# Optimization experiments

Measured on AMD Instinct MI355X. Metric: run time of the kernel, lower is better.

## Reference

```python
import jax, jax.numpy as jnp
import numpy as np

H, DK, DV, CHUNK = 4, 256, 256, 32
MIN_FLOOR, MAX_FLOOR, TEMP_MIN = 0.01, 0.1, 0.5


def _silu(x):
    return x * jax.nn.sigmoid(x)


def _causal_dw_conv(x_bcl, w_ck):
    # depthwise causal 1-D conv: x (b, C, L), w (C, K)
    K = w_ck.shape[-1]
    return jax.lax.conv_general_dilated(
        x_bcl, w_ck[:, None, :], window_strides=(1,), padding=[(K - 1, 0)],
        feature_group_count=x_bcl.shape[1])


def _l2norm(x):
    return x * jax.lax.rsqrt(jnp.sum(x * x, axis=-1, keepdims=True) + 1e-6)


def _delta_rule_chunkwise(q, k, v, beta, chunk=CHUNK):
    # q,k: (b,h,L,dk)  v: (b,h,L,dv)  beta: (b,h,L); L divisible by chunk
    b, h, L, dk = q.shape
    dv = v.shape[-1]
    n = L // chunk
    q = _l2norm(q)
    k = _l2norm(k)
    v = v * beta[..., None]
    kb = k * beta[..., None]
    qc, kc, vc, kbc = (t.reshape(b, h, n, chunk, -1) for t in (q, k, v, kb))
    # in-chunk inverse: the torch row loop computes (I + tril(k_beta k^T, -1))^{-1}
    A = jnp.einsum('bhncd,bhned->bhnce', kbc, kc)
    eye = jnp.eye(chunk, dtype=q.dtype)
    T = eye + jnp.tril(A, -1)
    inv = jax.scipy.linalg.solve_triangular(
        T, jnp.broadcast_to(eye, T.shape), lower=True, unit_diagonal=True)
    u = inv @ vc      # (b,h,n,c,dv)
    w = inv @ kbc     # (b,h,n,c,dk)
    strict = jnp.triu(jnp.ones((chunk, chunk), dtype=bool), 1)

    def step(S, xs):
        q_i, k_i, u_i, w_i = xs
        att = jnp.where(strict, 0.0, jnp.einsum('bhcd,bhed->bhce', q_i, k_i))
        u_adj = u_i - jnp.einsum('bhck,bhkd->bhcd', w_i, S)
        o = jnp.einsum('bhck,bhkd->bhcd', q_i, S) + att @ u_adj
        S = S + jnp.einsum('bhck,bhcd->bhkd', k_i, u_adj)
        return S, o

    mv = lambda t: jnp.moveaxis(t, 2, 0)  # chunks to scan axis
    S0 = jnp.zeros((b, h, dk, dv), dtype=q.dtype)
    S, outs = jax.lax.scan(step, S0, (mv(qc), mv(kc), mv(u), mv(w)))
    out = jnp.moveaxis(outs, 0, 2).reshape(b, h, L, dv)
    return out, S


def _fir(x, filt):
    # x: (b,l,h,d), filt: (h,d,K) depthwise causal FIR per (head, channel)
    b, l, h, d = x.shape
    xc = x.transpose(0, 2, 3, 1).reshape(b, h * d, l)
    y = _causal_dw_conv(xc, filt.reshape(h * d, -1))
    return y.reshape(b, h, d, l).transpose(0, 3, 1, 2)


def setup_inputs() -> dict:
    key = jax.random.key(0)
    ks = iter(jax.random.split(key, 32))
    B, L, D = 4, 2048, 1024
    kd, vd = H * DK, H * DV
    rn = lambda shp, s=0.02: jax.random.normal(next(ks), shp, jnp.float32) * s
    fir = lambda K: (jnp.zeros((H, DV, K), jnp.float32).at[..., -1].set(1.0)
                     + 0.01 * jax.random.normal(next(ks), (H, DV, K), jnp.float32))
    return dict(
        hidden_states=jax.random.normal(next(ks), (B, L, D), jnp.float32),
        Wq=rn((D, kd)), Wk=rn((D, kd)), Wv=rn((D, vd)),
        q_conv_w=rn((kd, 4), 0.3), k_conv_w=rn((kd, 4), 0.3), v_conv_w=rn((vd, 4), 0.3),
        Wb=rn((D, H)),
        fir_w3=fir(3), fir_w7=fir(7), fir_w15=fir(15), fir_w31=fir(31),
        router_W1=rn((D + DV * H * 5, 2 * D)), router_b1=jnp.zeros((2 * D,), jnp.float32),
        router_W2=rn((2 * D, H * 5)), router_b2=jnp.zeros((H * 5,), jnp.float32),
        id_gate_W=rn((D, H)), id_gate_b=jnp.full((H,), 2.0, jnp.float32),
        log_tau=jnp.zeros((H,), jnp.float32),
        o_norm_w=jnp.ones((DV,), jnp.float32),
        Wo=rn((vd, D)))


def reference(hidden_states, Wq, Wk, Wv, q_conv_w, k_conv_w, v_conv_w, Wb,
              fir_w3, fir_w7, fir_w15, fir_w31,
              router_W1, router_b1, router_W2, router_b2,
              id_gate_W, id_gate_b, log_tau, o_norm_w, Wo):
    B, L, D = hidden_states.shape
    conv = lambda x, w: _silu(_causal_dw_conv(x.transpose(0, 2, 1), w)).transpose(0, 2, 1)
    q = conv(hidden_states @ Wq, q_conv_w).reshape(B, L, H, DK)
    k = conv(hidden_states @ Wk, k_conv_w).reshape(B, L, H, DK)
    v_direct = conv(hidden_states @ Wv, v_conv_w).reshape(B, L, H, DV)
    beta = jax.nn.sigmoid(hidden_states @ Wb)  # (B,L,H)
    delta_out, _ = _delta_rule_chunkwise(
        q.transpose(0, 2, 1, 3), k.transpose(0, 2, 1, 3),
        v_direct.transpose(0, 2, 1, 3), beta.transpose(0, 2, 1))
    delta_out = delta_out.transpose(0, 2, 1, 3)  # (B,L,H,DV)
    paths = [_fir(v_direct, f) for f in (fir_w3, fir_w7, fir_w15, fir_w31)] + [delta_out]
    # token-adaptive value/context split
    p_value = jax.nn.sigmoid(hidden_states @ id_gate_W + id_gate_b)  # (B,L,H)
    floor_tok = MIN_FLOOR + (MAX_FLOOR - MIN_FLOOR) * (1.0 - p_value)
    p_value_adj = (1.0 - floor_tok) * p_value
    context_mass = 1.0 - p_value_adj
    # router over [hidden, all context paths]
    router_in = jnp.concatenate(
        [hidden_states] + [p.reshape(B, L, H * DV) for p in paths], axis=-1)
    hmid = jax.nn.gelu(router_in @ router_W1 + router_b1, approximate=False)
    logits = (hmid @ router_W2 + router_b2).reshape(B, L, H, 5)
    tau = jnp.maximum(jnp.exp(log_tau), TEMP_MIN)  # (H,)
    probs = jax.nn.softmax(logits / tau[:, None], axis=-1)
    ctx = sum(probs[..., i:i + 1] * paths[i] for i in range(5))
    o = context_mass[..., None] * ctx + p_value_adj[..., None] * v_direct
    # per-head RMSNorm then output projection
    o = o * jax.lax.rsqrt(jnp.mean(o * o, axis=-1, keepdims=True) + 1e-5) * o_norm_w
    return o.reshape(B, L, H * DV) @ Wo
```

## Files before the change

kernel.cpp:

```cpp
#include <hip/hip_runtime.h>
#include <math.h>

#define NTOK   8192
#define LSEQ   2048
#define NCHUNK 64

typedef short bhalf8 __attribute__((ext_vector_type(8)));
typedef float floatx4 __attribute__((ext_vector_type(4)));

__device__ inline ushort f2bf(float f) {
  uint u = __float_as_uint(f);
  u += 0x7FFFu + ((u >> 16) & 1u);
  return (ushort)(u >> 16);
}
__device__ inline float bf2f(ushort h) {
  return __uint_as_float(((uint)h) << 16);
}

#define GLD_LDS16(g, s) __builtin_amdgcn_global_load_lds(                      \
    (const __attribute__((address_space(1))) void*)(g),                        \
    (__attribute__((address_space(3))) void*)(s), 16, 0, 0)

__global__ __launch_bounds__(256)
void cvt_bf16(const float* __restrict__ x, ushort* __restrict__ y, int n8) {
  int i = blockIdx.x * 256 + threadIdx.x;
  if (i >= n8) return;
  const float4* xp = (const float4*)x;
  float4 a = xp[2 * i], b = xp[2 * i + 1];
  uint4 o;
  o.x = (uint)f2bf(a.x) | ((uint)f2bf(a.y) << 16);
  o.y = (uint)f2bf(a.z) | ((uint)f2bf(a.w) << 16);
  o.z = (uint)f2bf(b.x) | ((uint)f2bf(b.y) << 16);
  o.w = (uint)f2bf(b.z) | ((uint)f2bf(b.w) << 16);
  ((uint4*)y)[i] = o;
}

__global__ __launch_bounds__(256)
void cvt_t(const float* __restrict__ x, ushort* __restrict__ y, int R, int C) {
  __shared__ float tile[32][33];
  int r0 = blockIdx.y * 32, c0 = blockIdx.x * 32;
  int tr = threadIdx.x >> 5;
  int tc = threadIdx.x & 31;
  #pragma unroll
  for (int rr = tr; rr < 32; rr += 8)
    tile[rr][tc] = x[(size_t)(r0 + rr) * C + c0 + tc];
  __syncthreads();
  #pragma unroll
  for (int rr = tr; rr < 32; rr += 8)
    y[(size_t)(c0 + rr) * R + r0 + tc] = f2bf(tile[tc][rr]);
}

template<int ACC>
__global__ __launch_bounds__(256)
void gemm_bf(const ushort* __restrict__ A, const ushort* __restrict__ BT,
             float* __restrict__ C, int K, int lda, int ldbt, int ldc) {
  __shared__ ushort Asm[128 * 32];
  __shared__ ushort Bsm[128 * 32];
  const int t = threadIdx.x;
  const int w = t >> 6, l = t & 63;
  const int m0 = blockIdx.y * 128, n0 = blockIdx.x * 128;
  const int wr = w >> 1, wc = w & 1;
  const int srow = l >> 2;
  const int sgc  = (l & 3) ^ ((l >> 3) & 3);
  const int ridx = (l & 15) * 32 + (((l >> 4) ^ ((l >> 1) & 3)) * 8);

  floatx4 acc[4][4];
  #pragma unroll
  for (int i = 0; i < 4; i++)
    #pragma unroll
    for (int j = 0; j < 4; j++)
      #pragma unroll
      for (int r = 0; r < 4; r++) acc[i][j][r] = 0.f;

  for (int k0 = 0; k0 < K; k0 += 32) {
    __syncthreads();
    #pragma unroll
    for (int j = 0; j < 2; j++) {
      int sub = w * 2 + j;
      GLD_LDS16(A + (size_t)(m0 + sub * 16 + srow) * lda + k0 + sgc * 8,
                Asm + sub * 512);
      GLD_LDS16(BT + (size_t)(n0 + sub * 16 + srow) * ldbt + k0 + sgc * 8,
                Bsm + sub * 512);
    }
    __syncthreads();
    bhalf8 af[4], bf_[4];
    #pragma unroll
    for (int i = 0; i < 4; i++)
      af[i] = *(const bhalf8*)&Asm[(wr * 4 + i) * 512 + ridx];
    #pragma unroll
    for (int j = 0; j < 4; j++)
      bf_[j] = *(const bhalf8*)&Bsm[(wc * 4 + j) * 512 + ridx];
    #pragma unroll
    for (int i = 0; i < 4; i++)
      #pragma unroll
      for (int j = 0; j < 4; j++)
        acc[i][j] = __builtin_amdgcn_mfma_f32_16x16x32_bf16(af[i], bf_[j],
                                                            acc[i][j], 0, 0, 0);
  }
  const int crow = (l >> 4) * 4;
  const int ccol = l & 15;
  #pragma unroll
  for (int i = 0; i < 4; i++)
    #pragma unroll
    for (int j = 0; j < 4; j++) {
      float* cp = &C[(size_t)(m0 + wr * 64 + i * 16 + crow) * ldc +
                     n0 + wc * 64 + j * 16 + ccol];
      #pragma unroll
      for (int r = 0; r < 4; r++) {
        if (ACC) cp[(size_t)r * ldc] += acc[i][j][r];
        else     cp[(size_t)r * ldc]  = acc[i][j][r];
      }
    }
}

struct APtrs { const ushort* p[6]; };

__global__ __launch_bounds__(256)
void gemm_router(APtrs ap, const ushort* __restrict__ BT,
                 const float* __restrict__ bias, float* __restrict__ C) {
  __shared__ ushort Asm[128 * 32];
  __shared__ ushort Bsm[128 * 32];
  const int t = threadIdx.x;
  const int w = t >> 6, l = t & 63;
  const int m0 = blockIdx.y * 128, n0 = blockIdx.x * 128;
  const int wr = w >> 1, wc = w & 1;
  const int srow = l >> 2;
  const int sgc  = (l & 3) ^ ((l >> 3) & 3);
  const int ridx = (l & 15) * 32 + (((l >> 4) ^ ((l >> 1) & 3)) * 8);

  floatx4 acc[4][4];
  #pragma unroll
  for (int i = 0; i < 4; i++)
    #pragma unroll
    for (int j = 0; j < 4; j++)
      #pragma unroll
      for (int r = 0; r < 4; r++) acc[i][j][r] = 0.f;

  for (int k0 = 0; k0 < 6144; k0 += 32) {
    const ushort* Abase = ap.p[k0 >> 10];
    const int kk = k0 & 1023;
    __syncthreads();
    #pragma unroll
    for (int j = 0; j < 2; j++) {
      int sub = w * 2 + j;
      GLD_LDS16(Abase + (size_t)(m0 + sub * 16 + srow) * 1024 + kk + sgc * 8,
                Asm + sub * 512);
      GLD_LDS16(BT + (size_t)(n0 + sub * 16 + srow) * 6144 + k0 + sgc * 8,
                Bsm + sub * 512);
    }
    __syncthreads();
    bhalf8 af[4], bf_[4];
    #pragma unroll
    for (int i = 0; i < 4; i++)
      af[i] = *(const bhalf8*)&Asm[(wr * 4 + i) * 512 + ridx];
    #pragma unroll
    for (int j = 0; j < 4; j++)
      bf_[j] = *(const bhalf8*)&Bsm[(wc * 4 + j) * 512 + ridx];
    #pragma unroll
    for (int i = 0; i < 4; i++)
      #pragma unroll
      for (int j = 0; j < 4; j++)
        acc[i][j] = __builtin_amdgcn_mfma_f32_16x16x32_bf16(af[i], bf_[j],
                                                            acc[i][j], 0, 0, 0);
  }
  const int crow = (l >> 4) * 4;
  const int ccol = l & 15;
  #pragma unroll
  for (int i = 0; i < 4; i++)
    #pragma unroll
    for (int j = 0; j < 4; j++) {
      const int col = n0 + wc * 64 + j * 16 + ccol;
      const float bb = bias[col];
      float* cp = &C[(size_t)(m0 + wr * 64 + i * 16 + crow) * 1024 + col];
      #pragma unroll
      for (int r = 0; r < 4; r++) {
        float x = acc[i][j][r] + bb;
        cp[(size_t)r * 1024] = 0.5f * x * (1.f + erff(x * 0.70710678118654752f));
      }
    }
}

__global__ __launch_bounds__(256)
void conv4_silu(const float* __restrict__ x, const float* __restrict__ w,
                float* __restrict__ y) {
  int idx = blockIdx.x * 256 + threadIdx.x;
  int c = idx & 1023;
  int bl = idx >> 10;
  int l = bl & (LSEQ - 1);
  float w0 = w[c * 4 + 0], w1 = w[c * 4 + 1], w2 = w[c * 4 + 2], w3 = w[c * 4 + 3];
  float acc = x[idx] * w3;
  if (l >= 1) acc += x[idx - 1024] * w2;
  if (l >= 2) acc += x[idx - 2048] * w1;
  if (l >= 3) acc += x[idx - 3072] * w0;
  y[idx] = acc / (1.f + expf(-acc));
}

__global__ __launch_bounds__(256)
void pack_fir(const float* __restrict__ f3w, const float* __restrict__ f7w,
              const float* __restrict__ f15w, const float* __restrict__ f31w,
              float* __restrict__ fwTp) {
  int i = blockIdx.x * 256 + threadIdx.x;
  if (i >= 57344) return;
  int row = i >> 10, c = i & 1023;
  float val;
  if (row < 3)       val = f3w[c * 3 + row];
  else if (row < 10) val = f7w[c * 7 + (row - 3)];
  else if (row < 25) val = f15w[c * 15 + (row - 10)];
  else               val = f31w[c * 31 + (row - 25)];
  fwTp[i] = val;
}

__global__ __launch_bounds__(256)
void fir_all(const float* __restrict__ v, const float* __restrict__ fwTp,
             ushort* __restrict__ y3, ushort* __restrict__ y7,
             ushort* __restrict__ y15, ushort* __restrict__ y31) {
  int idx = blockIdx.x * 256 + threadIdx.x;
  int c = idx & 1023;
  int l = (idx >> 10) & (LSEQ - 1);
  float a3 = 0.f, a7 = 0.f, a15 = 0.f, a31 = 0.f;
  #pragma unroll
  for (int back = 30; back >= 0; back--) {
    float x = (l >= back) ? v[idx - back * 1024] : 0.f;
    a31 += x * fwTp[(25 + 30 - back) * 1024 + c];
    if (back <= 14) a15 += x * fwTp[(10 + 14 - back) * 1024 + c];
    if (back <= 6)  a7  += x * fwTp[(3 + 6 - back) * 1024 + c];
    if (back <= 2)  a3  += x * fwTp[(2 - back) * 1024 + c];
  }
  y3[idx]  = f2bf(a3);
  y7[idx]  = f2bf(a7);
  y15[idx] = f2bf(a15);
  y31[idx] = f2bf(a31);
}

__global__ __launch_bounds__(256)
void beta_pv(const float* __restrict__ hs, const float* __restrict__ Wb,
             const float* __restrict__ idW, const float* __restrict__ idb,
             float* __restrict__ beta, float* __restrict__ pv) {
  int tok = blockIdx.x;
  int h = threadIdx.x >> 6;
  int lane = threadIdx.x & 63;
  const float* hrow = hs + (size_t)tok * 1024;
  float s1 = 0.f, s2 = 0.f;
  #pragma unroll
  for (int j = 0; j < 16; j++) {
    int d = lane + j * 64;
    float hv = hrow[d];
    s1 += hv * Wb[d * 4 + h];
    s2 += hv * idW[d * 4 + h];
  }
  #pragma unroll
  for (int off = 32; off; off >>= 1) {
    s1 += __shfl_down(s1, off);
    s2 += __shfl_down(s2, off);
  }
  if (lane == 0) {
    beta[tok * 4 + h] = 1.f / (1.f + expf(-s1));
    pv[tok * 4 + h] = 1.f / (1.f + expf(-(s2 + idb[h])));
  }
}

__global__ __launch_bounds__(256)
void l2norm_qk(float* __restrict__ q, float* __restrict__ k) {
  int tok = blockIdx.x;
  int h = threadIdx.x >> 6;
  int lane = threadIdx.x & 63;
  size_t base = (size_t)tok * 1024 + h * 256 + lane * 4;
  {
    float4* p = (float4*)(q + base);
    float4 v = *p;
    float ss = v.x * v.x + v.y * v.y + v.z * v.z + v.w * v.w;
    #pragma unroll
    for (int off = 32; off; off >>= 1) ss += __shfl_xor(ss, off);
    float sc = rsqrtf(ss + 1e-6f);
    v.x *= sc; v.y *= sc; v.z *= sc; v.w *= sc;
    *p = v;
  }
  {
    float4* p = (float4*)(k + base);
    float4 v = *p;
    float ss = v.x * v.x + v.y * v.y + v.z * v.z + v.w * v.w;
    #pragma unroll
    for (int off = 32; off; off >>= 1) ss += __shfl_xor(ss, off);
    float sc = rsqrtf(ss + 1e-6f);
    v.x *= sc; v.y *= sc; v.z *= sc; v.w *= sc;
    *p = v;
  }
}

__global__ __launch_bounds__(256)
void chunk_prep(const float* __restrict__ q, const float* __restrict__ k,
                const float* __restrict__ v, const float* __restrict__ beta,
                ushort* __restrict__ attf, float* __restrict__ ub,
                ushort* __restrict__ wfb, ushort* __restrict__ qfb,
                ushort* __restrict__ ktb) {
  __shared__ float kbuf[32 * 260];
  __shared__ float qbuf[32 * 260];
  __shared__ float Am[32 * 32];
  __shared__ float bet[32];
  const int t = threadIdx.x;
  const int blk = blockIdx.x;
  const int n = blk & 63, bh = blk >> 6;
  const int h = bh & 3, b = bh >> 2;
  const size_t rowbase = (size_t)b * LSEQ + n * 32;
  const int cbase = h * 256;
  const int srow = t >> 6, scol = (t & 63) * 4;
  const size_t fb = (size_t)blk * 8192;

  #pragma unroll
  for (int rep = 0; rep < 8; rep++) {
    int r = rep * 4 + srow;
    *(float4*)&kbuf[r * 260 + scol] =
        *(const float4*)&k[(rowbase + r) * 1024 + cbase + scol];
    *(float4*)&qbuf[r * 260 + scol] =
        *(const float4*)&q[(rowbase + r) * 1024 + cbase + scol];
  }
  if (t < 32) bet[t] = beta[(rowbase + t) * 4 + h];
  __syncthreads();

  #pragma unroll
  for (int e = 0; e < 4; e++) {
    int idx = t + e * 256;
    int i = idx >> 5, jc = idx & 31;
    float da = 0.f, dq = 0.f;
    for (int d0 = 0; d0 < 256; d0 += 4) {
      float4 kj = *(float4*)&kbuf[jc * 260 + d0];
      float4 ki = *(float4*)&kbuf[i * 260 + d0];
      float4 qi = *(float4*)&qbuf[i * 260 + d0];
      da += ki.x * kj.x + ki.y * kj.y + ki.z * kj.z + ki.w * kj.w;
      dq += qi.x * kj.x + qi.y * kj.y + qi.z * kj.z + qi.w * kj.w;
    }
    Am[i * 32 + jc] = (jc < i) ? bet[i] * da : 0.f;
    float av = (jc <= i) ? dq : 0.f;
    attf[(size_t)blk * 1024 + (i >> 4) * 512 +
         ((i & 15) + ((jc >> 3) & 3) * 16) * 8 + (jc & 7)] = f2bf(av);
  }
  __syncthreads();

  #pragma unroll
  for (int cg = 0; cg < 4; cg++) {
    bhalf8 pk;
    #pragma unroll
    for (int j = 0; j < 8; j++)
      pk[j] = (short)f2bf(kbuf[(cg * 8 + j) * 260 + t]);
    *(bhalf8*)&ktb[fb + (t >> 4) * 512 + ((t & 15) + cg * 16) * 8] = pk;
  }

  #pragma unroll 1
  for (int i = 0; i < 32; i++) {
    float val = bet[i] * kbuf[i * 260 + t];
    for (int j = 0; j < i; j++) val -= Am[i * 32 + j] * kbuf[j * 260 + t];
    kbuf[i * 260 + t] = val;
  }
  __syncthreads();

  #pragma unroll
  for (int rep = 0; rep < 4; rep++) {
    int p = rep * 256 + t;
    int c = p & 31, dk8 = p >> 5;
    size_t pos = fb + ((size_t)(dk8 >> 2) * 2 + (c >> 4)) * 512 +
                 ((c & 15) + (dk8 & 3) * 16) * 8;
    bhalf8 pw, pq;
    #pragma unroll
    for (int j = 0; j < 8; j++) {
      pw[j] = (short)f2bf(kbuf[c * 260 + dk8 * 8 + j]);
      pq[j] = (short)f2bf(qbuf[c * 260 + dk8 * 8 + j]);
    }
    *(bhalf8*)&wfb[pos] = pw;
    *(bhalf8*)&qfb[pos] = pq;
  }
  __syncthreads();

  #pragma unroll
  for (int rep = 0; rep < 8; rep++) {
    int r = rep * 4 + srow;
    *(float4*)&qbuf[r * 260 + scol] =
        *(const float4*)&v[(rowbase + r) * 1024 + cbase + scol];
  }
  __syncthreads();
  #pragma unroll 1
  for (int i = 0; i < 32; i++) {
    float val = bet[i] * qbuf[i * 260 + t];
    for (int j = 0; j < i; j++) val -= Am[i * 32 + j] * qbuf[j * 260 + t];
    qbuf[i * 260 + t] = val;
  }
  for (int j = 0; j < 32; j++)
    ub[(rowbase + j) * 1024 + cbase + t] = qbuf[j * 260 + t];
}

__global__ __launch_bounds__(256)
void delta_scan(const ushort* __restrict__ wfb, const ushort* __restrict__ qfb,
                const ushort* __restrict__ ktb, const ushort* __restrict__ attf,
                const float* __restrict__ ub, ushort* __restrict__ outb) {
  __shared__ ushort wS[8192];
  __shared__ ushort qS[8192];
  __shared__ ushort kTS[8192];
  __shared__ ushort attS[1024];
  __shared__ ushort SbT[16 * 264];
  __shared__ ushort uaT[16 * 40];
  __shared__ float pbufW[4 * 544];
  __shared__ float pbufQ[4 * 544];
  __shared__ float oacc[544];
  const int t = threadIdx.x;
  const int w = t >> 6, l = t & 63;
  const int col16 = l & 15, g = l >> 4;
  const int blk = blockIdx.x;
  const int dsl = blk & 15, bh = blk >> 4;
  const int h = bh & 3, b = bh >> 2;
  const int dbase = h * 256 + dsl * 16;

  floatx4 S_acc[4];
  #pragma unroll
  for (int m = 0; m < 4; m++)
    #pragma unroll
    for (int r = 0; r < 4; r++) S_acc[m][r] = 0.f;

  for (int n = 0; n < NCHUNK; n++) {
    const size_t cb = ((size_t)(bh * 64 + n)) * 8192;
    const size_t ab = ((size_t)(bh * 64 + n)) * 1024;
    const size_t rowbase = (size_t)b * LSEQ + n * 32;

    #pragma unroll
    for (int m = 0; m < 4; m++) {
      uint lo = (uint)f2bf(S_acc[m][0]) | ((uint)f2bf(S_acc[m][1]) << 16);
      uint hi = (uint)f2bf(S_acc[m][2]) | ((uint)f2bf(S_acc[m][3]) << 16);
      uint2 pk; pk.x = lo; pk.y = hi;
      *(uint2*)&SbT[col16 * 264 + w * 64 + m * 16 + g * 4] = pk;
    }
    #pragma unroll
    for (int i = 0; i < 4; i++) {
      GLD_LDS16(wfb + cb + (w * 4 + i) * 512 + l * 8, &wS[(w * 4 + i) * 512]);
      GLD_LDS16(qfb + cb + (w * 4 + i) * 512 + l * 8, &qS[(w * 4 + i) * 512]);
      GLD_LDS16(ktb + cb + (w * 4 + i) * 512 + l * 8, &kTS[(w * 4 + i) * 512]);
    }
    if (w == 2) {
      GLD_LDS16(attf + ab + l * 8, &attS[0]);
      GLD_LDS16(attf + ab + 512 + l * 8, &attS[512]);
    }
    float u0 = ub[(rowbase + (t >> 4)) * 1024 + dbase + (t & 15)];
    float u1 = ub[(rowbase + 16 + (t >> 4)) * 1024 + dbase + (t & 15)];
    __syncthreads();

    floatx4 pw0, pw1, pq0, pq1;
    #pragma unroll
    for (int r = 0; r < 4; r++) { pw0[r] = 0.f; pw1[r] = 0.f; pq0[r] = 0.f; pq1[r] = 0.f; }
    #pragma unroll
    for (int s = 0; s < 2; s++) {
      const int koff = w * 2 + s;
      bhalf8 sb = *(const bhalf8*)&SbT[col16 * 264 + koff * 32 + g * 8];
      bhalf8 wa0 = *(const bhalf8*)&wS[((koff * 2 + 0) * 64 + l) * 8];
      bhalf8 wa1 = *(const bhalf8*)&wS[((koff * 2 + 1) * 64 + l) * 8];
      bhalf8 qa0 = *(const bhalf8*)&qS[((koff * 2 + 0) * 64 + l) * 8];
      bhalf8 qa1 = *(const bhalf8*)&qS[((koff * 2 + 1) * 64 + l) * 8];
      pw0 = __builtin_amdgcn_mfma_f32_16x16x32_bf16(wa0, sb, pw0, 0, 0, 0);
      pw1 = __builtin_amdgcn_mfma_f32_16x16x32_bf16(wa1, sb, pw1, 0, 0, 0);
      pq0 = __builtin_amdgcn_mfma_f32_16x16x32_bf16(qa0, sb, pq0, 0, 0, 0);
      pq1 = __builtin_amdgcn_mfma_f32_16x16x32_bf16(qa1, sb, pq1, 0, 0, 0);
    }
    #pragma unroll
    for (int r = 0; r < 4; r++) {
      pbufW[w * 544 + (g * 4 + r) * 17 + col16] = pw0[r];
      pbufW[w * 544 + (16 + g * 4 + r) * 17 + col16] = pw1[r];
      pbufQ[w * 544 + (g * 4 + r) * 17 + col16] = pq0[r];
      pbufQ[w * 544 + (16 + g * 4 + r) * 17 + col16] = pq1[r];
    }
    __syncthreads();

    {
      const int row = t >> 4, c2 = t & 15;
      const int i0 = row * 17 + c2, i1 = (row + 16) * 17 + c2;
      float wsA = pbufW[i0] + pbufW[544 + i0] + pbufW[1088 + i0] + pbufW[1632 + i0];
      float wsB = pbufW[i1] + pbufW[544 + i1] + pbufW[1088 + i1] + pbufW[1632 + i1];
      float qsA = pbufQ[i0] + pbufQ[544 + i0] + pbufQ[1088 + i0] + pbufQ[1632 + i0];
      float qsB = pbufQ[i1] + pbufQ[544 + i1] + pbufQ[1088 + i1] + pbufQ[1632 + i1];
      oacc[i0] = qsA;
      oacc[i1] = qsB;
      uaT[c2 * 40 + row] = f2bf(u0 - wsA);
      uaT[c2 * 40 + row + 16] = f2bf(u1 - wsB);
    }
    __syncthreads();

    bhalf8 uB = *(const bhalf8*)&uaT[col16 * 40 + g * 8];
    #pragma unroll
    for (int m = 0; m < 4; m++) {
      bhalf8 ka = *(const bhalf8*)&kTS[((w * 4 + m) * 64 + l) * 8];
      S_acc[m] = __builtin_amdgcn_mfma_f32_16x16x32_bf16(ka, uB, S_acc[m], 0, 0, 0);
    }
    if (w < 2) {
      floatx4 z;
      #pragma unroll
      for (int r = 0; r < 4; r++) z[r] = 0.f;
      bhalf8 aa = *(const bhalf8*)&attS[(w * 64 + l) * 8];
      floatx4 oat = __builtin_amdgcn_mfma_f32_16x16x32_bf16(aa, uB, z, 0, 0, 0);
      #pragma unroll
      for (int r = 0; r < 4; r++) {
        int row = w * 16 + g * 4 + r;
        float ov = oacc[row * 17 + col16] + oat[r];
        outb[(rowbase + row) * 1024 + dbase + col16] = f2bf(ov);
      }
    }
    __syncthreads();
  }
}

template<int FIRST>
__global__ __launch_bounds__(256)
void logits_acc(const float* __restrict__ hmid, const float* __restrict__ W2,
                const float* __restrict__ b2, float* __restrict__ logits) {
  __shared__ float hrow[1024];
  __shared__ float part[8][20];
  int tok = blockIdx.x, t = threadIdx.x;
  ((float4*)hrow)[t] = ((const float4*)(hmid + (size_t)tok * 1024))[t];
  __syncthreads();
  if (t < 160) {
    int col = t % 20, seg = t / 20;
    float acc = 0.f;
    for (int kk = 0; kk < 128; kk++) {
      int k2 = seg * 128 + kk;
      acc += hrow[k2] * W2[(size_t)k2 * 20 + col];
    }
    part[seg][col] = acc;
  }
  __syncthreads();
  if (t < 20) {
    float s = 0.f;
    #pragma unroll
    for (int g = 0; g < 8; g++) s += part[g][t];
    if (FIRST) logits[(size_t)tok * 20 + t] = b2[t] + s;
    else       logits[(size_t)tok * 20 + t] += s;
  }
}

__global__ __launch_bounds__(256)
void softmax_probs(const float* __restrict__ logits, const float* __restrict__ ltau,
                   float* __restrict__ probs) {
  int idx = blockIdx.x * 256 + threadIdx.x;
  int tok = idx >> 2, h = idx & 3;
  float tau = expf(ltau[h]);
  tau = tau < 0.5f ? 0.5f : tau;
  float x[5]; float m = -1e30f;
  #pragma unroll
  for (int i = 0; i < 5; i++) {
    x[i] = logits[(size_t)tok * 20 + h * 5 + i] / tau;
    m = fmaxf(m, x[i]);
  }
  float s = 0.f;
  #pragma unroll
  for (int i = 0; i < 5; i++) { x[i] = expf(x[i] - m); s += x[i]; }
  float inv = 1.f / s;
  #pragma unroll
  for (int i = 0; i < 5; i++) probs[(size_t)tok * 20 + h * 5 + i] = x[i] * inv;
}

__global__ __launch_bounds__(256)
void mix_rms(const ushort* __restrict__ f3, const ushort* __restrict__ f7,
             const ushort* __restrict__ f15, const ushort* __restrict__ f31,
             const ushort* __restrict__ dlt, const float* __restrict__ v,
             const float* __restrict__ probs, const float* __restrict__ pv,
             const float* __restrict__ onw, ushort* __restrict__ omix) {
  int tok = blockIdx.x;
  int h = threadIdx.x >> 6;
  int lane = threadIdx.x & 63;
  size_t base = (size_t)tok * 1024 + h * 256 + lane * 4;
  const float* pp = probs + (size_t)tok * 20 + h * 5;
  float p0 = pp[0], p1 = pp[1], p2 = pp[2], p3 = pp[3], p4 = pp[4];
  float pvv = pv[tok * 4 + h];
  float floor_tok = 0.01f + 0.09f * (1.f - pvv);
  float pa = (1.f - floor_tok) * pvv;
  float cm = 1.f - pa;
  ushort4 a4 = *(const ushort4*)&f3[base];
  ushort4 b4 = *(const ushort4*)&f7[base];
  ushort4 c4 = *(const ushort4*)&f15[base];
  ushort4 d4 = *(const ushort4*)&f31[base];
  ushort4 e4 = *(const ushort4*)&dlt[base];
  float4 vv = *(const float4*)&v[base];
  float av[4] = {bf2f(a4.x), bf2f(a4.y), bf2f(a4.z), bf2f(a4.w)};
  float bv[4] = {bf2f(b4.x), bf2f(b4.y), bf2f(b4.z), bf2f(b4.w)};
  float cv[4] = {bf2f(c4.x), bf2f(c4.y), bf2f(c4.z), bf2f(c4.w)};
  float dv[4] = {bf2f(d4.x), bf2f(d4.y), bf2f(d4.z), bf2f(d4.w)};
  float ev[4] = {bf2f(e4.x), bf2f(e4.y), bf2f(e4.z), bf2f(e4.w)};
  float vvv[4] = {vv.x, vv.y, vv.z, vv.w};
  float o[4];
  #pragma unroll
  for (int j = 0; j < 4; j++)
    o[j] = cm * (p0 * av[j] + p1 * bv[j] + p2 * cv[j] + p3 * dv[j] + p4 * ev[j]) +
           pa * vvv[j];
  float ss = o[0]*o[0] + o[1]*o[1] + o[2]*o[2] + o[3]*o[3];
  #pragma unroll
  for (int off = 32; off; off >>= 1) ss += __shfl_xor(ss, off);
  float sc = rsqrtf(ss * (1.f / 256.f) + 1e-5f);
  float4 wn = *(const float4*)&onw[lane * 4];
  ushort4 res;
  res.x = f2bf(o[0] * sc * wn.x); res.y = f2bf(o[1] * sc * wn.y);
  res.z = f2bf(o[2] * sc * wn.z); res.w = f2bf(o[3] * sc * wn.w);
  *(ushort4*)&omix[base] = res;
}

extern "C" void kernel_launch(void* const* d_in, const int* in_sizes, int n_in,
                              void* d_out, int out_size, void* d_ws, size_t ws_size,
                              hipStream_t stream) {
  const float* hs  = (const float*)d_in[0];
  const float* Wq  = (const float*)d_in[1];
  const float* Wk  = (const float*)d_in[2];
  const float* Wv  = (const float*)d_in[3];
  const float* qcw = (const float*)d_in[4];
  const float* kcw = (const float*)d_in[5];
  const float* vcw = (const float*)d_in[6];
  const float* Wb  = (const float*)d_in[7];
  const float* f3w = (const float*)d_in[8];
  const float* f7w = (const float*)d_in[9];
  const float* f15w= (const float*)d_in[10];
  const float* f31w= (const float*)d_in[11];
  const float* rW1 = (const float*)d_in[12];
  const float* rb1 = (const float*)d_in[13];
  const float* rW2 = (const float*)d_in[14];
  const float* rb2 = (const float*)d_in[15];
  const float* igW = (const float*)d_in[16];
  const float* igb = (const float*)d_in[17];
  const float* ltau= (const float*)d_in[18];
  const float* onw = (const float*)d_in[19];
  const float* Wo  = (const float*)d_in[20];
  float* out = (float*)d_out;
  float* ws  = (float*)d_ws;

  float* pre    = ws;
  float* qb     = ws +  8388608;
  float* kb     = ws + 16777216;
  float* vb     = ws + 25165824;
  float* ub     = ws + 33554432;
  float* wbuf   = ws + 41943040;
  float* dlt    = ws + 50331648;
  float* fwTp   = ws + 58720256;
  float* beta   = ws + 59768832;
  float* pv     = ws + 59801600;
  float* logits = ws + 59834368;
  float* probs  = ws + 59998208;

  ushort* hs_bf1 = (ushort*)ub;
  ushort* WqT    = (ushort*)(ub + 4194304);
  ushort* WkT    = WqT + 1048576;
  ushort* WvT    = WkT + 1048576;
  ushort* ktb    = (ushort*)pre;
  ushort* attfb  = (ushort*)(pre + 4194304);
  ushort* wfb    = (ushort*)wbuf;
  ushort* qfb    = (ushort*)(wbuf + 4194304);
  ushort* f3b    = (ushort*)ub;
  ushort* f7b    = (ushort*)(ub + 4194304);
  ushort* f15b   = (ushort*)wbuf;
  ushort* f31b   = (ushort*)(wbuf + 4194304);
  ushort* dltb   = (ushort*)dlt;
  ushort* omixb  = (ushort*)(dlt + 4194304);
  ushort* hs_bf2 = (ushort*)kb;
  ushort* WoT    = (ushort*)(kb + 4194304);
  ushort* W1T    = (ushort*)qb;
  float*  hmid   = pre;

  dim3 blk(256);
  dim3 gg(8, 64);

  cvt_bf16<<<4096, blk, 0, stream>>>(hs, hs_bf1, 1048576);
  cvt_t<<<dim3(32, 32), blk, 0, stream>>>(Wq, WqT, 1024, 1024);
  cvt_t<<<dim3(32, 32), blk, 0, stream>>>(Wk, WkT, 1024, 1024);
  cvt_t<<<dim3(32, 32), blk, 0, stream>>>(Wv, WvT, 1024, 1024);
  gemm_bf<0><<<gg, blk, 0, stream>>>(hs_bf1, WqT, pre, 1024, 1024, 1024, 1024);
  conv4_silu<<<32768, blk, 0, stream>>>(pre, qcw, qb);
  gemm_bf<0><<<gg, blk, 0, stream>>>(hs_bf1, WkT, pre, 1024, 1024, 1024, 1024);
  conv4_silu<<<32768, blk, 0, stream>>>(pre, kcw, kb);
  gemm_bf<0><<<gg, blk, 0, stream>>>(hs_bf1, WvT, pre, 1024, 1024, 1024, 1024);
  conv4_silu<<<32768, blk, 0, stream>>>(pre, vcw, vb);

  beta_pv<<<8192, blk, 0, stream>>>(hs, Wb, igW, igb, beta, pv);
  l2norm_qk<<<8192, blk, 0, stream>>>(qb, kb);

  chunk_prep<<<1024, blk, 0, stream>>>(qb, kb, vb, beta, attfb, ub, wfb, qfb, ktb);
  delta_scan<<<256, blk, 0, stream>>>(wfb, qfb, ktb, attfb, ub, dltb);

  pack_fir<<<224, blk, 0, stream>>>(f3w, f7w, f15w, f31w, fwTp);
  fir_all<<<32768, blk, 0, stream>>>(vb, fwTp, f3b, f7b, f15b, f31b);

  cvt_bf16<<<4096, blk, 0, stream>>>(hs, hs_bf2, 1048576);
  cvt_t<<<dim3(64, 192), blk, 0, stream>>>(rW1, W1T, 6144, 2048);
  cvt_t<<<dim3(32, 32), blk, 0, stream>>>(Wo, WoT, 1024, 1024);

  APtrs ap;
  ap.p[0] = hs_bf2; ap.p[1] = f3b; ap.p[2] = f7b;
  ap.p[3] = f15b;   ap.p[4] = f31b; ap.p[5] = dltb;
  for (int nh = 0; nh < 2; nh++) {
    gemm_router<<<gg, blk, 0, stream>>>(ap, W1T + (size_t)nh * 1024 * 6144,
                                        rb1 + nh * 1024, hmid);
    if (nh == 0) logits_acc<1><<<8192, blk, 0, stream>>>(hmid, rW2, rb2, logits);
    else         logits_acc<0><<<8192, blk, 0, stream>>>(hmid, rW2 + (size_t)1024 * 20, rb2, logits);
  }
  softmax_probs<<<128, blk, 0, stream>>>(logits, ltau, probs);

  mix_rms<<<8192, blk, 0, stream>>>(f3b, f7b, f15b, f31b, dltb, vb, probs, pv,
                                    onw, omixb);
  gemm_bf<0><<<gg, blk, 0, stream>>>(omixb, WoT, out, 1024, 1024, 1024, 1024);
}
```

Before: 1.224 ms.

## Merge router GEMM halves into one launch with bf16 hidden output and XCD-aware block mapping

Replaces the two router-GEMM-plus-logits passes with a single 16x64-block GEMM that covers all 2048 hidden units, writes the GELU output as bf16, and feeds one logits kernel that reads the full bf16 row. Router blocks are remapped so that consecutive block IDs on the same XCD share A rows, which should improve L2 reuse. Launch count and hidden-activation traffic drop, in exchange for bf16 rounding of the router hidden layer. gemm_bf also gets a block-index remap, which is effectively the identity.

```diff
diff --git a/kernel.cpp b/kernel.cpp
--- a/kernel.cpp
+++ b/kernel.cpp
@@ -58,7 +58,8 @@
   __shared__ ushort Bsm[128 * 32];
   const int t = threadIdx.x;
   const int w = t >> 6, l = t & 63;
-  const int m0 = blockIdx.y * 128, n0 = blockIdx.x * 128;
+  const int bid = blockIdx.y * 8 + blockIdx.x;
+  const int m0 = (bid >> 3) * 128, n0 = (bid & 7) * 128;
   const int wr = w >> 1, wc = w & 1;
   const int srow = l >> 2;
   const int sgc  = (l & 3) ^ ((l >> 3) & 3);
@@ -117,12 +118,14 @@
 
 __global__ __launch_bounds__(256)
 void gemm_router(APtrs ap, const ushort* __restrict__ BT,
-                 const float* __restrict__ bias, float* __restrict__ C) {
+                 const float* __restrict__ bias, ushort* __restrict__ Ch) {
   __shared__ ushort Asm[128 * 32];
   __shared__ ushort Bsm[128 * 32];
   const int t = threadIdx.x;
   const int w = t >> 6, l = t & 63;
-  const int m0 = blockIdx.y * 128, n0 = blockIdx.x * 128;
+  const int bid = blockIdx.y * 16 + blockIdx.x;
+  const int xcd = bid & 7, idx = bid >> 3;
+  const int m0 = (idx >> 1) * 128, n0 = (xcd * 2 + (idx & 1)) * 128;
   const int wr = w >> 1, wc = w & 1;
   const int srow = l >> 2;
   const int sgc  = (l & 3) ^ ((l >> 3) & 3);
@@ -171,11 +174,12 @@
     for (int j = 0; j < 4; j++) {
       const int col = n0 + wc * 64 + j * 16 + ccol;
       const float bb = bias[col];
-      float* cp = &C[(size_t)(m0 + wr * 64 + i * 16 + crow) * 1024 + col];
+      ushort* cp = &Ch[(size_t)(m0 + wr * 64 + i * 16 + crow) * 2048 + col];
       #pragma unroll
       for (int r = 0; r < 4; r++) {
         float x = acc[i][j][r] + bb;
-        cp[(size_t)r * 1024] = 0.5f * x * (1.f + erff(x * 0.70710678118654752f));
+        cp[(size_t)r * 2048] =
+            f2bf(0.5f * x * (1.f + erff(x * 0.70710678118654752f)));
       }
     }
 }
@@ -502,31 +506,34 @@
   }
 }
 
-template<int FIRST>
-__global__ __launch_bounds__(256)
-void logits_acc(const float* __restrict__ hmid, const float* __restrict__ W2,
+__global__ __launch_bounds__(256)
+void logits_one(const ushort* __restrict__ hmid, const float* __restrict__ W2,
                 const float* __restrict__ b2, float* __restrict__ logits) {
-  __shared__ float hrow[1024];
+  __shared__ float hrow[2048];
   __shared__ float part[8][20];
   int tok = blockIdx.x, t = threadIdx.x;
-  ((float4*)hrow)[t] = ((const float4*)(hmid + (size_t)tok * 1024))[t];
+  {
+    uint4 hv = ((const uint4*)(hmid + (size_t)tok * 2048))[t];
+    const ushort* hp = (const ushort*)&hv;
+    #pragma unroll
+    for (int j = 0; j < 8; j++) hrow[t * 8 + j] = bf2f(hp[j]);
+  }
   __syncthreads();
   if (t < 160) {
     int col = t % 20, seg = t / 20;
     float acc = 0.f;
-    for (int kk = 0; kk < 128; kk++) {
-      int k2 = seg * 128 + kk;
+    for (int kk = 0; kk < 256; kk++) {
+      int k2 = seg * 256 + kk;
       acc += hrow[k2] * W2[(size_t)k2 * 20 + col];
     }
     part[seg][col] = acc;
   }
   __syncthreads();
   if (t < 20) {
-    float s = 0.f;
+    float s = b2[t];
     #pragma unroll
     for (int g = 0; g < 8; g++) s += part[g][t];
-    if (FIRST) logits[(size_t)tok * 20 + t] = b2[t] + s;
-    else       logits[(size_t)tok * 20 + t] += s;
+    logits[(size_t)tok * 20 + t] = s;
   }
 }
 
@@ -652,10 +659,11 @@
   ushort* hs_bf2 = (ushort*)kb;
   ushort* WoT    = (ushort*)(kb + 4194304);
   ushort* W1T    = (ushort*)qb;
-  float*  hmid   = pre;
+  ushort* hmidb  = (ushort*)pre;
 
   dim3 blk(256);
   dim3 gg(8, 64);
+  dim3 gg2(16, 64);
 
   cvt_bf16<<<4096, blk, 0, stream>>>(hs, hs_bf1, 1048576);
   cvt_t<<<dim3(32, 32), blk, 0, stream>>>(Wq, WqT, 1024, 1024);
@@ -684,12 +692,8 @@
   APtrs ap;
   ap.p[0] = hs_bf2; ap.p[1] = f3b; ap.p[2] = f7b;
   ap.p[3] = f15b;   ap.p[4] = f31b; ap.p[5] = dltb;
-  for (int nh = 0; nh < 2; nh++) {
-    gemm_router<<<gg, blk, 0, stream>>>(ap, W1T + (size_t)nh * 1024 * 6144,
-                                        rb1 + nh * 1024, hmid);
-    if (nh == 0) logits_acc<1><<<8192, blk, 0, stream>>>(hmid, rW2, rb2, logits);
-    else         logits_acc<0><<<8192, blk, 0, stream>>>(hmid, rW2 + (size_t)1024 * 20, rb2, logits);
-  }
+  gemm_router<<<gg2, blk, 0, stream>>>(ap, W1T, rb1, hmidb);
+  logits_one<<<8192, blk, 0, stream>>>(hmidb, rW2, rb2, logits);
   softmax_probs<<<128, blk, 0, stream>>>(logits, ltau, probs);
 
   mix_rms<<<8192, blk, 0, stream>>>(f3b, f7b, f15b, f31b, dltb, vb, probs, pv,
```

Result: faster. 1.199 ms (-2.0%).
